# Kernel optimization log

Measured on AMD Instinct MI355X. Metric: run time of the kernel, lower is better.

Reference implementation:

```python
import jax, jax.numpy as jnp
import numpy as np
import math

B, S, D, H = 4, 2048, 1024, 16
DK = D // H


def setup_inputs() -> dict:
    key = jax.random.key(0)
    ks = jax.random.split(key, 11)
    s = 1.0 / math.sqrt(D)
    inp = {
        "query": jax.random.normal(ks[0], (B, S, D), jnp.float32),
        "key": jax.random.normal(ks[1], (B, S, D), jnp.float32),
        "value": jax.random.normal(ks[2], (B, S, D), jnp.float32),
        # torch nn.Linear params: weight [out,in], bias [out]
        "Wq": jax.random.uniform(ks[3], (D, D), jnp.float32, -s, s),
        "bq": jax.random.uniform(ks[4], (D,), jnp.float32, -s, s),
        "Wk": jax.random.uniform(ks[5], (D, D), jnp.float32, -s, s),
        "bk": jax.random.uniform(ks[6], (D,), jnp.float32, -s, s),
        "Wv": jax.random.uniform(ks[7], (D, D), jnp.float32, -s, s),
        "bv": jax.random.uniform(ks[8], (D,), jnp.float32, -s, s),
        "Wo": jax.random.uniform(ks[9], (D, D), jnp.float32, -s, s),
        "bo": jax.random.uniform(ks[10], (D,), jnp.float32, -s, s),
    }
    return inp


def _split_heads(x):
    # [B,S,D] -> [B,H,S,DK]
    return x.reshape(B, S, H, DK).transpose(0, 2, 1, 3)


def reference(query, key, value, Wq, bq, Wk, bk, Wv, bv, Wo, bo):
    q = _split_heads(query @ Wq.T + bq)
    k = _split_heads(key @ Wk.T + bk)
    v = _split_heads(value @ Wv.T + bv)
    scores = jnp.einsum("bhqd,bhkd->bhqk", q, k) / math.sqrt(DK)
    p = jax.nn.softmax(scores, axis=-1)  # dropout p=0 -> identity
    x = jnp.einsum("bhqk,bhkd->bhqd", p, v)
    x = x.transpose(0, 2, 1, 3).reshape(B, S, D)
    return x @ Wo.T + bo
```

## Files before the change

kernel.cpp:

```cpp
#include <hip/hip_runtime.h>
#include <hip/hip_bf16.h>


typedef __attribute__((ext_vector_type(8))) short bf16x8;
typedef __attribute__((ext_vector_type(4))) float f32x4;

static __device__ __forceinline__ unsigned short f2bf(float f) {
  union { __hip_bfloat16 h; unsigned short u; } cv;
  cv.h = __float2bfloat16(f);
  return cv.u;
}

static __device__ __forceinline__ unsigned int pack2bf(float a, float b) {
  union { __hip_bfloat162 h; unsigned int u; } cv;
  cv.h = __float22bfloat162_rn(float2{a, b});
  return cv.u;
}

static __device__ __forceinline__ void pl32swap(unsigned int& a, unsigned int& b) {
  asm volatile("v_permlane32_swap_b32 %0, %1" : "+v"(a), "+v"(b));
}
static __device__ __forceinline__ void pl16swap(unsigned int& a, unsigned int& b) {
  asm volatile("v_permlane16_swap_b32 %0, %1" : "+v"(a), "+v"(b));
}

static __device__ __forceinline__ void gload_lds16(const void* g, void* l) {
  __builtin_amdgcn_global_load_lds(
      (const __attribute__((address_space(1))) unsigned int*)g,
      (__attribute__((address_space(3))) unsigned int*)l, 16, 0, 0);
}

template<int NJ>
struct CvtJobs { const float* in[NJ]; unsigned short* out[NJ]; int n; };

template<int NJ>
__global__ __launch_bounds__(256) void cvt_batch(CvtJobs<NJ> jobs) {
  const float* __restrict__ in = jobs.in[blockIdx.y];
  unsigned short* __restrict__ out = jobs.out[blockIdx.y];
  int i = (blockIdx.x * 256 + threadIdx.x) * 4;
  if (i + 3 < jobs.n) {
    float4 v = *(const float4*)(in + i);
    ushort4 o;
    o.x = f2bf(v.x); o.y = f2bf(v.y); o.z = f2bf(v.z); o.w = f2bf(v.w);
    *(ushort4*)(out + i) = o;
  }
}

template<int MODE>
__global__ __launch_bounds__(256) void gemm_bt(const unsigned short* __restrict__ A_,
                                               const unsigned short* __restrict__ Bw_,
                                               const float* __restrict__ bias,
                                               const float* __restrict__ bias1,
                                               void* __restrict__ outp,
                                               int M, int N, int K) {
  __shared__ unsigned short As[128 * 32];
  __shared__ unsigned short Bs[128 * 32];
  const int tid = threadIdx.x;
  const int w = tid >> 6, lane = tid & 63;
  const int wr = w >> 1, wc = w & 1;
  const int fr = lane & 15, fg = lane >> 4;

  const unsigned short* A = A_;
  const unsigned short* Bw = Bw_;
  float scale = 1.f;
  unsigned short* out16 = (unsigned short*)outp;
  if (MODE == 4) {
    const int z = blockIdx.z;
    A += (size_t)z * (8192 * 1024);
    Bw += (size_t)z * (1024 * 1024);
    out16 += (size_t)z * (8192 * 1024);
    if (z == 0) scale = 0.125f; else bias = bias1;
  }

  int bx, by;
  if (MODE != 2) {
    const int nwg = gridDim.x * gridDim.y;
    const int lin = blockIdx.y * gridDim.x + blockIdx.x;
    const int nb = (lin & 7) * (nwg >> 3) + (lin >> 3);
    bx = nb % gridDim.x; by = nb / gridDim.x;
  } else {
    bx = blockIdx.x; by = blockIdx.y;
  }
  const int m0 = by * 128, n0 = bx * 128;

  f32x4 acc[4][4] = {};
  const int e0 = (w * 2) * 512 + lane * 8;

  for (int kt = 0; kt < K; kt += 32) {
#pragma unroll
    for (int i = 0; i < 2; ++i) {
      const int e = e0 + i * 512;
      const int row = e >> 5, kk = e & 31;
      gload_lds16(A + (size_t)(m0 + row) * K + kt + kk, (void*)(As + e));
      gload_lds16(Bw + (size_t)(n0 + row) * K + kt + kk, (void*)(Bs + e));
    }
    __syncthreads();
    bf16x8 af[4], bfr[4];
#pragma unroll
    for (int m = 0; m < 4; ++m)
      af[m] = *(const bf16x8*)(As + (wr * 64 + m * 16 + fr) * 32 + fg * 8);
#pragma unroll
    for (int n = 0; n < 4; ++n)
      bfr[n] = *(const bf16x8*)(Bs + (wc * 64 + n * 16 + fr) * 32 + fg * 8);
#pragma unroll
    for (int m = 0; m < 4; ++m)
#pragma unroll
      for (int n = 0; n < 4; ++n)
        acc[m][n] = __builtin_amdgcn_mfma_f32_16x16x32_bf16(af[m], bfr[n], acc[m][n], 0, 0, 0);
    __syncthreads();
  }

#pragma unroll
  for (int m = 0; m < 4; ++m) {
#pragma unroll
    for (int n = 0; n < 4; ++n) {
      const int gn = n0 + wc * 64 + n * 16 + fr;
#pragma unroll
      for (int r = 0; r < 4; ++r) {
        const int gm = m0 + wr * 64 + m * 16 + fg * 4 + r;
        float val = acc[m][n][r];
        if (MODE == 2) val += bias[gm]; else val += bias[gn];
        if (MODE == 4) {
          val *= scale;
          size_t idx = ((size_t)((gm >> 11) * 16 + (gn >> 6)) * 2048 + (gm & 2047)) * 64 + (gn & 63);
          out16[idx] = f2bf(val);
        } else if (MODE == 2) {
          size_t idx = ((size_t)((gn >> 11) * 16 + (gm >> 6)) * 64 + (gm & 63)) * 2048 + (gn & 2047);
          out16[idx] = f2bf(val);
        } else {
          ((float*)outp)[(size_t)gm * N + gn] = val;
        }
      }
    }
  }
}

__global__ __launch_bounds__(256, 2) void attn_kernel(const unsigned short* __restrict__ Qh,
                                                      const unsigned short* __restrict__ Kh,
                                                      const unsigned short* __restrict__ Vt,
                                                      unsigned short* __restrict__ Xa) {
  const int S = 2048, DK = 64;
  __shared__ float Ssum[4][64];
  const int tid = threadIdx.x;
  const int w = tid >> 6, lane = tid & 63;
  const int fr = lane & 15, fg = lane >> 4;

  const int bid = blockIdx.x;
  const int xcd = bid & 7, slot = bid >> 3;
  const int bh = xcd * 8 + (slot >> 3);
  const int qblk = slot & 7;
  const int q0 = qblk * 256 + w * 64;

  const unsigned short* Qp = Qh + (size_t)bh * S * DK;
  const unsigned short* Kp = Kh + (size_t)bh * S * DK;
  const unsigned short* Vp = Vt + (size_t)bh * DK * S;

  bf16x8 qf[4][2];
#pragma unroll
  for (int nt = 0; nt < 4; ++nt)
#pragma unroll
    for (int ks = 0; ks < 2; ++ks)
      qf[nt][ks] = *(const bf16x8*)(Qp + (size_t)(q0 + nt * 16 + fr) * DK + ks * 32 + fg * 8);

  f32x4 xacc[4][4] = {};
  float psum[4] = {0.f, 0.f, 0.f, 0.f};

  for (int kv = 0; kv < S; kv += 64) {
    bf16x8 kf[4][2];
#pragma unroll
    for (int mt = 0; mt < 4; ++mt)
#pragma unroll
      for (int ks = 0; ks < 2; ++ks)
        kf[mt][ks] = *(const bf16x8*)(Kp + (size_t)(kv + mt * 16 + fr) * DK + ks * 32 + fg * 8);
    bf16x8 vf[4][2];
#pragma unroll
    for (int dn = 0; dn < 4; ++dn)
#pragma unroll
      for (int ks = 0; ks < 2; ++ks)
        vf[dn][ks] = *(const bf16x8*)(Vp + (size_t)(dn * 16 + fr) * S + kv + ks * 32 + fg * 8);

#pragma unroll
    for (int nt = 0; nt < 4; ++nt) {
      f32x4 sc[4];
#pragma unroll
      for (int mt = 0; mt < 4; ++mt) {
        sc[mt] = __builtin_amdgcn_mfma_f32_16x16x32_bf16(kf[mt][0], qf[nt][0],
                                                         (f32x4){0.f, 0.f, 0.f, 0.f}, 0, 0, 0);
        sc[mt] = __builtin_amdgcn_mfma_f32_16x16x32_bf16(kf[mt][1], qf[nt][1], sc[mt], 0, 0, 0);
      }
      unsigned int X[4][2];
      float ps = 0.f;
#pragma unroll
      for (int mt = 0; mt < 4; ++mt) {
        const float p0 = __expf(sc[mt][0]);
        const float p1 = __expf(sc[mt][1]);
        const float p2 = __expf(sc[mt][2]);
        const float p3 = __expf(sc[mt][3]);
        ps += (p0 + p1) + (p2 + p3);
        X[mt][0] = pack2bf(p0, p1);
        X[mt][1] = pack2bf(p2, p3);
      }
      psum[nt] += ps;

      union { unsigned int u[4]; bf16x8 b; } pa0, pa1;
      {
        unsigned int F0 = X[0][0], G0 = X[1][0]; pl32swap(F0, G0); pl16swap(F0, G0);
        unsigned int F1 = X[0][1], G1 = X[1][1]; pl32swap(F1, G1); pl16swap(F1, G1);
        pa0.u[0] = F0; pa0.u[1] = F1; pa0.u[2] = G0; pa0.u[3] = G1;
      }
      {
        unsigned int F0 = X[2][0], G0 = X[3][0]; pl32swap(F0, G0); pl16swap(F0, G0);
        unsigned int F1 = X[2][1], G1 = X[3][1]; pl32swap(F1, G1); pl16swap(F1, G1);
        pa1.u[0] = F0; pa1.u[1] = F1; pa1.u[2] = G0; pa1.u[3] = G1;
      }

#pragma unroll
      for (int dn = 0; dn < 4; ++dn)
        xacc[nt][dn] = __builtin_amdgcn_mfma_f32_16x16x32_bf16(pa0.b, vf[dn][0], xacc[nt][dn], 0, 0, 0);
#pragma unroll
      for (int dn = 0; dn < 4; ++dn)
        xacc[nt][dn] = __builtin_amdgcn_mfma_f32_16x16x32_bf16(pa1.b, vf[dn][1], xacc[nt][dn], 0, 0, 0);
    }
  }

#pragma unroll
  for (int nt = 0; nt < 4; ++nt) {
    psum[nt] += __shfl_xor(psum[nt], 16);
    psum[nt] += __shfl_xor(psum[nt], 32);
  }
  if (lane < 16) {
#pragma unroll
    for (int nt = 0; nt < 4; ++nt) Ssum[w][nt * 16 + lane] = psum[nt];
  }

  const int b = bh >> 4, h = bh & 15;
#pragma unroll
  for (int m = 0; m < 4; ++m) {
#pragma unroll
    for (int r = 0; r < 4; ++r) {
      const float inv = 1.f / Ssum[w][m * 16 + fg * 4 + r];
      const int s = q0 + m * 16 + fg * 4 + r;
      unsigned short* dst = Xa + ((size_t)(b * 2048 + s)) * 1024 + h * 64;
#pragma unroll
      for (int dn = 0; dn < 4; ++dn)
        dst[dn * 16 + fr] = f2bf(xacc[m][dn][r] * inv);
    }
  }
}

extern "C" void kernel_launch(void* const* d_in, const int* in_sizes, int n_in,
                              void* d_out, int out_size, void* d_ws, size_t ws_size,
                              hipStream_t stream) {
  (void)in_sizes; (void)n_in; (void)out_size;
  const float* q  = (const float*)d_in[0];
  const float* k  = (const float*)d_in[1];
  const float* v  = (const float*)d_in[2];
  const float* Wq = (const float*)d_in[3];
  const float* bq = (const float*)d_in[4];
  const float* Wk = (const float*)d_in[5];
  const float* bk = (const float*)d_in[6];
  const float* Wv = (const float*)d_in[7];
  const float* bv = (const float*)d_in[8];
  const float* Wo = (const float*)d_in[9];
  const float* bo = (const float*)d_in[10];
  float* out = (float*)d_out;

  const size_t XB = (size_t)8192 * 1024;
  const size_t WB = (size_t)1024 * 1024;
  const size_t need = (7 * XB + 4 * WB) * 2;
  if (ws_size < need) return;

  unsigned short* ws  = (unsigned short*)d_ws;
  unsigned short* xq  = ws;
  unsigned short* xk  = xq + XB;
  unsigned short* xv  = xk + XB;
  unsigned short* wqb = xv + XB;
  unsigned short* wkb = wqb + WB;
  unsigned short* wvb = wkb + WB;
  unsigned short* wob = wvb + WB;
  unsigned short* Qh  = wob + WB;
  unsigned short* Kh  = Qh + XB;
  unsigned short* Vt  = Kh + XB;
  unsigned short* Xa  = Vt + XB;

  CvtJobs<3> jx; jx.in[0] = q; jx.in[1] = k; jx.in[2] = v;
  jx.out[0] = xq; jx.out[1] = xk; jx.out[2] = xv; jx.n = (int)XB;
  cvt_batch<3><<<dim3(XB / 1024, 3), 256, 0, stream>>>(jx);
  CvtJobs<4> jw; jw.in[0] = Wq; jw.in[1] = Wk; jw.in[2] = Wv; jw.in[3] = Wo;
  jw.out[0] = wqb; jw.out[1] = wkb; jw.out[2] = wvb; jw.out[3] = wob; jw.n = (int)WB;
  cvt_batch<4><<<dim3(WB / 1024, 4), 256, 0, stream>>>(jw);

  gemm_bt<4><<<dim3(8, 64, 2), 256, 0, stream>>>(xq, wqb, bq, bk, Qh, 8192, 1024, 1024);
  gemm_bt<2><<<dim3(64, 8), 256, 0, stream>>>(wvb, xv, bv, nullptr, Vt, 1024, 8192, 1024);

  attn_kernel<<<dim3(512), 256, 0, stream>>>(Qh, Kh, Vt, Xa);

  gemm_bt<3><<<dim3(8, 64), 256, 0, stream>>>(Xa, wob, bo, nullptr, out, 8192, 1024, 1024);
}
```

Baseline: 393.7 us.

## Double-buffer K tiles, fold log2e into Q scale, use exp2 and setprio

After: 556.2 us. +41.3%, slower.

```diff
diff --git a/kernel.cpp b/kernel.cpp
--- a/kernel.cpp
+++ b/kernel.cpp
@@ -69,7 +69,8 @@
     A += (size_t)z * (8192 * 1024);
     Bw += (size_t)z * (1024 * 1024);
     out16 += (size_t)z * (8192 * 1024);
-    if (z == 0) scale = 0.125f; else bias = bias1;
+    if (z == 0) scale = 0.18033688011f;
+    else bias = bias1;
   }
 
   int bx, by;
@@ -160,42 +161,47 @@
   for (int nt = 0; nt < 4; ++nt)
 #pragma unroll
     for (int ks = 0; ks < 2; ++ks)
-      qf[nt][ks] = *(const bf16x8*)(Qp + (size_t)(q0 + nt * 16 + fr) * DK + ks * 32 + fg * 8);
+      qf[nt][ks] = __builtin_nontemporal_load(
+          (const bf16x8*)(Qp + (size_t)(q0 + nt * 16 + fr) * DK + ks * 32 + fg * 8));
 
   f32x4 xacc[4][4] = {};
   float psum[4] = {0.f, 0.f, 0.f, 0.f};
-
-  for (int kv = 0; kv < S; kv += 64) {
-    bf16x8 kf[4][2];
+  bf16x8 kfA[4][2], kfB[4][2], vf[4][2];
+
+  auto loadK = [&](bf16x8 (&kf)[4][2], int kv) {
 #pragma unroll
     for (int mt = 0; mt < 4; ++mt)
 #pragma unroll
       for (int ks = 0; ks < 2; ++ks)
         kf[mt][ks] = *(const bf16x8*)(Kp + (size_t)(kv + mt * 16 + fr) * DK + ks * 32 + fg * 8);
-    bf16x8 vf[4][2];
+  };
+  auto loadV = [&](int kv) {
 #pragma unroll
     for (int dn = 0; dn < 4; ++dn)
 #pragma unroll
       for (int ks = 0; ks < 2; ++ks)
         vf[dn][ks] = *(const bf16x8*)(Vp + (size_t)(dn * 16 + fr) * S + kv + ks * 32 + fg * 8);
-
+  };
+  auto compute = [&](bf16x8 (&kf)[4][2]) {
 #pragma unroll
     for (int nt = 0; nt < 4; ++nt) {
       f32x4 sc[4];
+      __builtin_amdgcn_s_setprio(1);
 #pragma unroll
       for (int mt = 0; mt < 4; ++mt) {
         sc[mt] = __builtin_amdgcn_mfma_f32_16x16x32_bf16(kf[mt][0], qf[nt][0],
                                                          (f32x4){0.f, 0.f, 0.f, 0.f}, 0, 0, 0);
         sc[mt] = __builtin_amdgcn_mfma_f32_16x16x32_bf16(kf[mt][1], qf[nt][1], sc[mt], 0, 0, 0);
       }
+      __builtin_amdgcn_s_setprio(0);
       unsigned int X[4][2];
       float ps = 0.f;
 #pragma unroll
       for (int mt = 0; mt < 4; ++mt) {
-        const float p0 = __expf(sc[mt][0]);
-        const float p1 = __expf(sc[mt][1]);
-        const float p2 = __expf(sc[mt][2]);
-        const float p3 = __expf(sc[mt][3]);
+        const float p0 = exp2f(sc[mt][0]);
+        const float p1 = exp2f(sc[mt][1]);
+        const float p2 = exp2f(sc[mt][2]);
+        const float p3 = exp2f(sc[mt][3]);
         ps += (p0 + p1) + (p2 + p3);
         X[mt][0] = pack2bf(p0, p1);
         X[mt][1] = pack2bf(p2, p3);
@@ -214,13 +220,25 @@
         pa1.u[0] = F0; pa1.u[1] = F1; pa1.u[2] = G0; pa1.u[3] = G1;
       }
 
+      __builtin_amdgcn_s_setprio(1);
 #pragma unroll
       for (int dn = 0; dn < 4; ++dn)
         xacc[nt][dn] = __builtin_amdgcn_mfma_f32_16x16x32_bf16(pa0.b, vf[dn][0], xacc[nt][dn], 0, 0, 0);
 #pragma unroll
       for (int dn = 0; dn < 4; ++dn)
         xacc[nt][dn] = __builtin_amdgcn_mfma_f32_16x16x32_bf16(pa1.b, vf[dn][1], xacc[nt][dn], 0, 0, 0);
+      __builtin_amdgcn_s_setprio(0);
     }
+  };
+
+  loadK(kfA, 0);
+  for (int kv = 0; kv < S; kv += 128) {
+    loadV(kv);
+    loadK(kfB, kv + 64);
+    compute(kfA);
+    loadV(kv + 64);
+    loadK(kfA, (kv + 128) & (S - 1));
+    compute(kfB);
   }
 
 #pragma unroll
@@ -243,7 +261,7 @@
       unsigned short* dst = Xa + ((size_t)(b * 2048 + s)) * 1024 + h * 64;
 #pragma unroll
       for (int dn = 0; dn < 4; ++dn)
-        dst[dn * 16 + fr] = f2bf(xacc[m][dn][r] * inv);
+        __builtin_nontemporal_store(f2bf(xacc[m][dn][r] * inv), dst + dn * 16 + fr);
     }
   }
 }
```

## Prefetch next K/V tile in registers, use exp2 and MFMA row sums

Applied to the files above, without the earlier changes.

Result: no change. 399.1 us (+1.4%).

```diff
diff --git a/kernel.cpp b/kernel.cpp
--- a/kernel.cpp
+++ b/kernel.cpp
@@ -69,7 +69,8 @@
     A += (size_t)z * (8192 * 1024);
     Bw += (size_t)z * (1024 * 1024);
     out16 += (size_t)z * (8192 * 1024);
-    if (z == 0) scale = 0.125f; else bias = bias1;
+    if (z == 0) scale = 0.18033688011f;
+    else bias = bias1;
   }
 
   int bx, by;
@@ -140,7 +141,6 @@
                                                       const unsigned short* __restrict__ Vt,
                                                       unsigned short* __restrict__ Xa) {
   const int S = 2048, DK = 64;
-  __shared__ float Ssum[4][64];
   const int tid = threadIdx.x;
   const int w = tid >> 6, lane = tid & 63;
   const int fr = lane & 15, fg = lane >> 4;
@@ -162,47 +162,55 @@
     for (int ks = 0; ks < 2; ++ks)
       qf[nt][ks] = *(const bf16x8*)(Qp + (size_t)(q0 + nt * 16 + fr) * DK + ks * 32 + fg * 8);
 
+  bf16x8 ones;
+#pragma unroll
+  for (int j = 0; j < 8; ++j) ones[j] = (short)0x3F80;
+
   f32x4 xacc[4][4] = {};
-  float psum[4] = {0.f, 0.f, 0.f, 0.f};
-
-  for (int kv = 0; kv < S; kv += 64) {
-    bf16x8 kf[4][2];
-#pragma unroll
-    for (int mt = 0; mt < 4; ++mt)
-#pragma unroll
-      for (int ks = 0; ks < 2; ++ks)
-        kf[mt][ks] = *(const bf16x8*)(Kp + (size_t)(kv + mt * 16 + fr) * DK + ks * 32 + fg * 8);
-    bf16x8 vf[4][2];
-#pragma unroll
-    for (int dn = 0; dn < 4; ++dn)
-#pragma unroll
-      for (int ks = 0; ks < 2; ++ks)
-        vf[dn][ks] = *(const bf16x8*)(Vp + (size_t)(dn * 16 + fr) * S + kv + ks * 32 + fg * 8);
-
+  f32x4 xsum[4] = {};
+
+  bf16x8 kf[4][2], vf[4][2];
+#pragma unroll
+  for (int mt = 0; mt < 4; ++mt)
+#pragma unroll
+    for (int ks = 0; ks < 2; ++ks)
+      kf[mt][ks] = *(const bf16x8*)(Kp + (size_t)(mt * 16 + fr) * DK + ks * 32 + fg * 8);
+#pragma unroll
+  for (int dn = 0; dn < 4; ++dn)
+#pragma unroll
+    for (int ks = 0; ks < 2; ++ks)
+      vf[dn][ks] = *(const bf16x8*)(Vp + (size_t)(dn * 16 + fr) * S + ks * 32 + fg * 8);
+
+  for (int t = 0; t < 32; ++t) {
+    const int kvn = ((t + 1) & 31) * 64;
 #pragma unroll
     for (int nt = 0; nt < 4; ++nt) {
       f32x4 sc[4];
+      __builtin_amdgcn_s_setprio(1);
 #pragma unroll
       for (int mt = 0; mt < 4; ++mt) {
         sc[mt] = __builtin_amdgcn_mfma_f32_16x16x32_bf16(kf[mt][0], qf[nt][0],
                                                          (f32x4){0.f, 0.f, 0.f, 0.f}, 0, 0, 0);
         sc[mt] = __builtin_amdgcn_mfma_f32_16x16x32_bf16(kf[mt][1], qf[nt][1], sc[mt], 0, 0, 0);
       }
+      __builtin_amdgcn_s_setprio(0);
+
+      if (nt == 3) {
+#pragma unroll
+        for (int mt = 0; mt < 4; ++mt)
+#pragma unroll
+          for (int ks = 0; ks < 2; ++ks)
+            kf[mt][ks] = *(const bf16x8*)(Kp + (size_t)(kvn + mt * 16 + fr) * DK + ks * 32 + fg * 8);
+      }
+
       unsigned int X[4][2];
-      float ps = 0.f;
 #pragma unroll
       for (int mt = 0; mt < 4; ++mt) {
-        const float p0 = __expf(sc[mt][0]);
-        const float p1 = __expf(sc[mt][1]);
-        const float p2 = __expf(sc[mt][2]);
-        const float p3 = __expf(sc[mt][3]);
-        ps += (p0 + p1) + (p2 + p3);
-        X[mt][0] = pack2bf(p0, p1);
-        X[mt][1] = pack2bf(p2, p3);
-      }
-      psum[nt] += ps;
-
-      union { unsigned int u[4]; bf16x8 b; } pa0, pa1;
+        X[mt][0] = pack2bf(exp2f(sc[mt][0]), exp2f(sc[mt][1]));
+        X[mt][1] = pack2bf(exp2f(sc[mt][2]), exp2f(sc[mt][3]));
+      }
+
+      union { unsigned int u[4]; bf16x8 v; } pa0, pa1;
       {
         unsigned int F0 = X[0][0], G0 = X[1][0]; pl32swap(F0, G0); pl16swap(F0, G0);
         unsigned int F1 = X[0][1], G1 = X[1][1]; pl32swap(F1, G1); pl16swap(F1, G1);
@@ -214,31 +222,37 @@
         pa1.u[0] = F0; pa1.u[1] = F1; pa1.u[2] = G0; pa1.u[3] = G1;
       }
 
+      __builtin_amdgcn_s_setprio(1);
 #pragma unroll
       for (int dn = 0; dn < 4; ++dn)
-        xacc[nt][dn] = __builtin_amdgcn_mfma_f32_16x16x32_bf16(pa0.b, vf[dn][0], xacc[nt][dn], 0, 0, 0);
+        xacc[nt][dn] = __builtin_amdgcn_mfma_f32_16x16x32_bf16(pa0.v, vf[dn][0], xacc[nt][dn], 0, 0, 0);
+      xsum[nt] = __builtin_amdgcn_mfma_f32_16x16x32_bf16(pa0.v, ones, xsum[nt], 0, 0, 0);
+      __builtin_amdgcn_s_setprio(0);
+      if (nt == 3) {
+#pragma unroll
+        for (int dn = 0; dn < 4; ++dn)
+          vf[dn][0] = *(const bf16x8*)(Vp + (size_t)(dn * 16 + fr) * S + kvn + fg * 8);
+      }
+      __builtin_amdgcn_s_setprio(1);
 #pragma unroll
       for (int dn = 0; dn < 4; ++dn)
-        xacc[nt][dn] = __builtin_amdgcn_mfma_f32_16x16x32_bf16(pa1.b, vf[dn][1], xacc[nt][dn], 0, 0, 0);
+        xacc[nt][dn] = __builtin_amdgcn_mfma_f32_16x16x32_bf16(pa1.v, vf[dn][1], xacc[nt][dn], 0, 0, 0);
+      xsum[nt] = __builtin_amdgcn_mfma_f32_16x16x32_bf16(pa1.v, ones, xsum[nt], 0, 0, 0);
+      __builtin_amdgcn_s_setprio(0);
+      if (nt == 3) {
+#pragma unroll
+        for (int dn = 0; dn < 4; ++dn)
+          vf[dn][1] = *(const bf16x8*)(Vp + (size_t)(dn * 16 + fr) * S + kvn + 32 + fg * 8);
+      }
     }
   }
 
-#pragma unroll
-  for (int nt = 0; nt < 4; ++nt) {
-    psum[nt] += __shfl_xor(psum[nt], 16);
-    psum[nt] += __shfl_xor(psum[nt], 32);
-  }
-  if (lane < 16) {
-#pragma unroll
-    for (int nt = 0; nt < 4; ++nt) Ssum[w][nt * 16 + lane] = psum[nt];
-  }
-
   const int b = bh >> 4, h = bh & 15;
 #pragma unroll
   for (int m = 0; m < 4; ++m) {
 #pragma unroll
     for (int r = 0; r < 4; ++r) {
-      const float inv = 1.f / Ssum[w][m * 16 + fg * 4 + r];
+      const float inv = 1.f / xsum[m][r];
       const int s = q0 + m * 16 + fg * 4 + r;
       unsigned short* dst = Xa + ((size_t)(b * 2048 + s)) * 1024 + h * 64;
 #pragma unroll
```
